# Optimization experiments

Hardware: AMD Instinct MI355X
Metric: run time of the kernel (lower is better)

## Reference

```python
import jax, jax.numpy as jnp
import numpy as np

N = 50000
E = 800000
H = 96
NUM_IN = 11
PE_DIM = 24
NUM_OUT = 1
NUM_LAYERS = 4
NUM_GRAPHS = 256


def _linear_params(key, d_in, d_out):
    k1, k2 = jax.random.split(key)
    bound = 1.0 / np.sqrt(d_in)
    w = jax.random.uniform(k1, (d_in, d_out), jnp.float32, -bound, bound)
    b = jax.random.uniform(k2, (d_out,), jnp.float32, -bound, bound)
    return w, b


def setup_inputs() -> dict:
    key = jax.random.key(0)
    ks = jax.random.split(key, 32)
    x = jax.random.normal(ks[0], (N, NUM_IN), jnp.float32)
    pos = jax.random.normal(ks[1], (N, 3), jnp.float32)
    pe = jax.random.normal(ks[2], (N, PE_DIM), jnp.float32)
    edge_index = jax.random.randint(ks[3], (2, E), 0, N, jnp.int64)
    batch = jnp.sort(jax.random.randint(ks[4], (N,), 0, NUM_GRAPHS, jnp.int64))
    embed_w1, embed_b1 = _linear_params(ks[5], NUM_IN + PE_DIM, H)
    embed_w2, embed_b2 = _linear_params(ks[6], H, H)
    # per-layer stacked params
    msg_w1 = []; msg_b1 = []; msg_w2 = []; msg_b2 = []
    upd_w1 = []; upd_b1 = []; upd_w2 = []; upd_b2 = []
    for l in range(NUM_LAYERS):
        w, b = _linear_params(ks[7 + l], 2 * H + 1, H); msg_w1.append(w); msg_b1.append(b)
        w, b = _linear_params(ks[11 + l], H, H); msg_w2.append(w); msg_b2.append(b)
        w, b = _linear_params(ks[15 + l], 2 * H, H); upd_w1.append(w); upd_b1.append(b)
        w, b = _linear_params(ks[19 + l], H, H); upd_w2.append(w); upd_b2.append(b)
    pre_w1, pre_b1 = _linear_params(ks[23], H, H)
    pre_w2, pre_b2 = _linear_params(ks[24], H, H)
    ro_w1, ro_b1 = _linear_params(ks[25], H, H)
    ro_w2, ro_b2 = _linear_params(ks[26], H, NUM_OUT)
    return {
        'x': x, 'pos': pos, 'pe': pe, 'edge_index': edge_index, 'batch': batch,
        'embed_w1': embed_w1, 'embed_b1': embed_b1, 'embed_w2': embed_w2, 'embed_b2': embed_b2,
        'msg_w1': jnp.stack(msg_w1), 'msg_b1': jnp.stack(msg_b1),
        'msg_w2': jnp.stack(msg_w2), 'msg_b2': jnp.stack(msg_b2),
        'upd_w1': jnp.stack(upd_w1), 'upd_b1': jnp.stack(upd_b1),
        'upd_w2': jnp.stack(upd_w2), 'upd_b2': jnp.stack(upd_b2),
        'pre_w1': pre_w1, 'pre_b1': pre_b1, 'pre_w2': pre_w2, 'pre_b2': pre_b2,
        'ro_w1': ro_w1, 'ro_b1': ro_b1, 'ro_w2': ro_w2, 'ro_b2': ro_b2,
    }


def _egnn_forward(x, pos, pe, edge_index, batch,
                  embed_w1, embed_b1, embed_w2, embed_b2,
                  msg_w1, msg_b1, msg_w2, msg_b2,
                  upd_w1, upd_b1, upd_w2, upd_b2,
                  pre_w1, pre_b1, pre_w2, pre_b2,
                  ro_w1, ro_b1, ro_w2, ro_b2):
    silu = jax.nn.silu
    send, rec = edge_index[0], edge_index[1]
    h = jnp.concatenate([x, pe], axis=-1)
    h = silu(h @ embed_w1 + embed_b1) @ embed_w2 + embed_b2  # [N,H]
    dist = jnp.linalg.norm(pos[send] - pos[rec], axis=1)[:, None]  # [E,1]
    for l in range(NUM_LAYERS):
        state = jnp.concatenate([h[send], h[rec], dist], axis=1)  # [E,2H+1]
        msg = silu(silu(state @ msg_w1[l] + msg_b1[l]) @ msg_w2[l] + msg_b2[l])  # [E,H]
        aggr = jax.ops.segment_sum(msg, rec, num_segments=h.shape[0])  # [N,H]
        upd_in = jnp.concatenate([h, aggr], axis=1)
        update = silu(upd_in @ upd_w1[l] + upd_b1[l]) @ upd_w2[l] + upd_b2[l]
        h = h + update
    h = silu(h @ pre_w1 + pre_b1) @ pre_w2 + pre_b2
    pooled = jax.ops.segment_sum(h, batch, num_segments=NUM_GRAPHS)  # [G,H]
    out = silu(pooled @ ro_w1 + ro_b1) @ ro_w2 + ro_b2  # [G,1]
    return jnp.squeeze(out)


def reference(x, pos, pe, edge_index, batch,
              embed_w1, embed_b1, embed_w2, embed_b2,
              msg_w1, msg_b1, msg_w2, msg_b2,
              upd_w1, upd_b1, upd_w2, upd_b2,
              pre_w1, pre_b1, pre_w2, pre_b2,
              ro_w1, ro_b1, ro_w2, ro_b2):
    return _egnn_forward(x, pos, pe, edge_index, batch,
                         embed_w1, embed_b1, embed_w2, embed_b2,
                         msg_w1, msg_b1, msg_w2, msg_b2,
                         upd_w1, upd_b1, upd_w2, upd_b2,
                         pre_w1, pre_b1, pre_w2, pre_b2,
                         ro_w1, ro_b1, ro_w2, ro_b2)
```

## Files before the change

kernel.cpp:

```cpp
#include <hip/hip_runtime.h>
#include <hip/hip_bf16.h>

#define HDIM 96
#define TILE 128

typedef __attribute__((ext_vector_type(8))) short  short8;
typedef __attribute__((ext_vector_type(4))) short  short4v;
typedef __attribute__((ext_vector_type(4))) float  float4v;
typedef __attribute__((ext_vector_type(4))) unsigned int uint4v;

static __device__ __forceinline__ short f2bf(float f){
    __hip_bfloat16 h = __float2bfloat16(f);
    return *reinterpret_cast<short*>(&h);
}
static __device__ __forceinline__ float bf2f(short s){
    unsigned u = ((unsigned)(unsigned short)s) << 16;
    return __uint_as_float(u);
}
static __device__ __forceinline__ float silu_f(float v){
    return v * __builtin_amdgcn_rcpf(1.0f + __expf(-v));
}

struct SwJob { const float* src; int ck; int ks; int ksrc; };
struct SwTable { SwJob j[22]; };

__global__ __launch_bounds__(256) void swizzle_kernel(SwTable T, short* __restrict__ dst, int total){
    int gid = blockIdx.x*256 + threadIdx.x;
    if (gid >= total) return;
    int ksg = gid / 3072;
    int e   = gid % 3072;
    const float* src = T.j[0].src; int k0 = 0, ksrc = 0;
    #pragma unroll
    for (int jj = 0; jj < 22; ++jj){
        int s = T.j[jj].ck;
        if (ksg >= s && ksg < s + T.j[jj].ks){ src = T.j[jj].src; k0 = (ksg - s)*32; ksrc = T.j[jj].ksrc; }
    }
    int nt   = e >> 9;
    int rem  = e & 511;
    int lane = rem >> 3;
    int jx   = rem & 7;
    int k = k0 + ((lane >> 4) << 3) + jx;
    int f = nt*16 + (lane & 15);
    float v = (k < ksrc) ? src[(size_t)k*HDIM + f] : 0.0f;
    dst[gid] = f2bf(v);
}

__global__ __launch_bounds__(256) void swizzle2_kernel(const float* __restrict__ msg_w1,
                                                       short* __restrict__ dst, int total){
    int gid = blockIdx.x*256 + threadIdx.x;
    if (gid >= total) return;
    int layer = gid / 18432;
    int e     = gid % 18432;
    int ksg = e / 6144;
    int rem = e % 6144;
    int nt   = rem >> 9;
    int r2   = rem & 511;
    int lane = r2 >> 3;
    int jx   = r2 & 7;
    int k = ksg*32 + ((lane >> 4) << 3) + jx;
    int f = nt*16 + (lane & 15);
    int row = (f < 96) ? k : (96 + k);
    int col = (f < 96) ? f : (f - 96);
    dst[gid] = f2bf(msg_w1[(size_t)layer*193*96 + (size_t)row*96 + col]);
}

__global__ __launch_bounds__(256) void hist_kernel(const int* __restrict__ rec, int* __restrict__ deg, int E){
    int e = blockIdx.x*256 + threadIdx.x;
    if (e < E) atomicAdd(&deg[rec[e]], 1);
}

__global__ __launch_bounds__(256) void scan_part(const int* __restrict__ deg, int* __restrict__ part, int N){
    __shared__ int red[256];
    const int t = threadIdx.x;
    int base = blockIdx.x*1024;
    int s = 0;
    #pragma unroll
    for (int j=0;j<4;j++){ int i = base + j*256 + t; s += (i<N)?deg[i]:0; }
    red[t]=s; __syncthreads();
    #pragma unroll
    for (int off=128; off>0; off>>=1){ if (t<off) red[t]+=red[t+off]; __syncthreads(); }
    if (t==0) part[blockIdx.x]=red[0];
}
__global__ void scan_top(int* __restrict__ part, int nb){
    if (threadIdx.x==0){ int run=0; for (int i=0;i<nb;i++){ int v=part[i]; part[i]=run; run+=v; } }
}
__global__ __launch_bounds__(256) void scan_final(const int* __restrict__ deg, const int* __restrict__ part,
                                                  int* __restrict__ cur, int N){
    __shared__ int tsum[256];
    const int t = threadIdx.x;
    int i0 = blockIdx.x*1024 + t*4;
    int a0 = (i0+0<N)?deg[i0+0]:0;
    int a1 = (i0+1<N)?deg[i0+1]:0;
    int a2 = (i0+2<N)?deg[i0+2]:0;
    int a3 = (i0+3<N)?deg[i0+3]:0;
    int s = a0+a1+a2+a3;
    tsum[t]=s; __syncthreads();
    #pragma unroll
    for (int off=1; off<256; off<<=1){
        int u = (t>=off)?tsum[t-off]:0;
        __syncthreads();
        tsum[t]+=u;
        __syncthreads();
    }
    int excl = tsum[t]-s + part[blockIdx.x];
    if (i0+0<N) cur[i0+0]=excl;
    if (i0+1<N) cur[i0+1]=excl+a0;
    if (i0+2<N) cur[i0+2]=excl+a0+a1;
    if (i0+3<N) cur[i0+3]=excl+a0+a1+a2;
}

__global__ __launch_bounds__(256) void scatter_kernel(
    const int* __restrict__ send, const int* __restrict__ rec, const float* __restrict__ pos,
    int* __restrict__ cur, int* __restrict__ send_s, int* __restrict__ rec_s,
    float* __restrict__ dist_s, int E)
{
    int e = blockIdx.x*256 + threadIdx.x;
    if (e >= E) return;
    int s = send[e], r = rec[e];
    int p = atomicAdd(&cur[r], 1);
    send_s[p] = s;
    rec_s[p]  = r;
    float dx = pos[3*s]   - pos[3*r];
    float dy = pos[3*s+1] - pos[3*r+1];
    float dz = pos[3*s+2] - pos[3*r+2];
    dist_s[p] = sqrtf(dx*dx + dy*dy + dz*dz);
}

__global__ __launch_bounds__(256,2) void msgpre_kernel(
    const short* __restrict__ hbf, const short* __restrict__ w1sr, const float* __restrict__ b1,
    short* __restrict__ SR, int N)
{
    __shared__ short stateS[TILE*104];
    const int t  = threadIdx.x;
    const int n0 = blockIdx.x * TILE;

    #pragma unroll
    for (int it = 0; it < 6; ++it) {
        int q = it*256 + t;
        int c = q % 12;
        int i = q / 12;
        int node = n0 + i;
        uint4v v = {0u,0u,0u,0u};
        if (node < N) v = *(const uint4v*)(hbf + (size_t)node*HDIM + c*8);
        *(uint4v*)(stateS + i*104 + c*8) = v;
    }
    __syncthreads();

    const int lane = t & 63;
    const int wv   = t >> 6;
    const int e_lo = wv * 32;
    const int col  = lane & 15;
    const int quad = lane >> 4;
    const int koff = quad * 8;
    const int frow = quad * 4;
    const float4v fzero = {0.f,0.f,0.f,0.f};

    float4v acc[2][12];
    #pragma unroll
    for (int i=0;i<2;i++)
      #pragma unroll
      for (int n=0;n<12;n++) acc[i][n] = fzero;

    const short8* w1f = (const short8*)w1sr;
    #pragma unroll
    for (int ks = 0; ks < 3; ++ks) {
        short8 bb0 = *(const short8*)(stateS + (e_lo+col)*104    + ks*32 + koff);
        short8 bb1 = *(const short8*)(stateS + (e_lo+16+col)*104 + ks*32 + koff);
        #pragma unroll
        for (int mt = 0; mt < 12; ++mt) {
            short8 a = w1f[(ks*12+mt)*64 + lane];
            acc[0][mt] = __builtin_amdgcn_mfma_f32_16x16x32_bf16(a, bb0, acc[0][mt], 0, 0, 0);
            acc[1][mt] = __builtin_amdgcn_mfma_f32_16x16x32_bf16(a, bb1, acc[1][mt], 0, 0, 0);
        }
    }
    float4v b1v[6];
    #pragma unroll
    for (int mt=0; mt<6; ++mt) b1v[mt] = *(const float4v*)(b1 + mt*16 + frow);

    #pragma unroll
    for (int et=0; et<2; ++et){
        int node = n0 + e_lo + et*16 + col;
        if (node < N) {
            size_t base = (size_t)node*192;
            #pragma unroll
            for (int mt=0; mt<12; ++mt){
                float4v o = acc[et][mt];
                if (mt < 6) { o[0]+=b1v[mt][0]; o[1]+=b1v[mt][1]; o[2]+=b1v[mt][2]; o[3]+=b1v[mt][3]; }
                short4v sv = {f2bf(o[0]), f2bf(o[1]), f2bf(o[2]), f2bf(o[3])};
                *(short4v*)(SR + base + mt*16 + frow) = sv;
            }
        }
    }
}

__global__ __launch_bounds__(256,3) void edge_kernel(
    const short* __restrict__ SR,
    const int* __restrict__ send_s, const int* __restrict__ rec_s, const float* __restrict__ dist_s,
    const float* __restrict__ w1r192,
    const short* __restrict__ w2sw, const float* __restrict__ b2,
    float* __restrict__ aggr, int E)
{
    __shared__ float msgS[TILE*100];
    __shared__ int   recS[TILE];
    __shared__ int   startIdxS[TILE+1];
    __shared__ int   wcntS[2];
    const int t  = threadIdx.x;
    const int e0 = blockIdx.x * TILE;

    if (t < TILE) {
        int e = e0 + t; if (e >= E) e = E - 1;
        recS[t] = rec_s[e];
    }
    __syncthreads();

    bool flag = false;
    if (t < TILE) flag = (t == 0) || (recS[t] != recS[t-1]);
    unsigned long long bmask = __ballot(flag ? 1 : 0);
    int pre = __popcll(bmask & ((1ull << (t & 63)) - 1ull));
    if (t < TILE && (t & 63) == 0) wcntS[t >> 6] = __popcll(bmask);
    __syncthreads();
    const int nseg = wcntS[0] + wcntS[1];
    if (flag) startIdxS[pre + ((t >> 6) ? wcntS[0] : 0)] = t;
    if (t == 0) startIdxS[nseg] = TILE;

    const int lane = t & 63;
    const int wv   = t >> 6;
    const int e_lo = wv * 32;
    const int col  = lane & 15;
    const int quad = lane >> 4;
    const int frow = quad * 4;
    const float4v fzero = {0.f,0.f,0.f,0.f};

    short8 frag[2][3];
    #pragma unroll
    for (int et=0; et<2; ++et){
        int ei = e_lo + et*16 + col;
        int ec = e0 + ei; if (ec >= E) ec = E - 1;
        int se = send_s[ec];
        int re = recS[ei];
        float d = dist_s[ec];
        #pragma unroll
        for (int ks=0; ks<3; ++ks){
            int f0 = ks*32 + quad*8;
            short8 S8 = *(const short8*)(SR + (size_t)se*192 + f0);
            short8 R8 = *(const short8*)(SR + (size_t)re*192 + 96 + f0);
            float4v wa = *(const float4v*)(w1r192 + f0);
            float4v wb = *(const float4v*)(w1r192 + f0 + 4);
            short8 fr;
            #pragma unroll
            for (int j=0;j<8;j++){
                float w = (j<4) ? wa[j] : wb[j-4];
                float v = bf2f(S8[j]) + bf2f(R8[j]) + d*w;
                fr[j] = f2bf(silu_f(v));
            }
            frag[et][ks] = fr;
        }
    }

    float4v acc2[2][6];
    #pragma unroll
    for (int i=0;i<2;i++)
      #pragma unroll
      for (int n=0;n<6;n++) acc2[i][n] = fzero;

    const short8* w2f = (const short8*)w2sw;
    #pragma unroll
    for (int ks = 0; ks < 3; ++ks) {
        #pragma unroll
        for (int mt = 0; mt < 6; ++mt) {
            short8 a = w2f[(ks*6+mt)*64 + lane];
            acc2[0][mt] = __builtin_amdgcn_mfma_f32_16x16x32_bf16(a, frag[0][ks], acc2[0][mt], 0, 0, 0);
            acc2[1][mt] = __builtin_amdgcn_mfma_f32_16x16x32_bf16(a, frag[1][ks], acc2[1][mt], 0, 0, 0);
        }
    }
    float4v b2v[6];
    #pragma unroll
    for (int mt=0; mt<6; ++mt) b2v[mt] = *(const float4v*)(b2 + mt*16 + frow);

    #pragma unroll
    for (int et=0; et<2; ++et){
        int e = e_lo + et*16 + col;
        bool valid = (e0 + e) < E;
        #pragma unroll
        for (int mt=0; mt<6; ++mt){
            float4v v;
            #pragma unroll
            for (int r=0;r<4;r++){
                float u = silu_f(acc2[et][mt][r] + b2v[mt][r]);
                v[r] = valid ? u : 0.0f;
            }
            *(float4v*)(msgS + e*100 + mt*16 + frow) = v;
        }
    }
    __syncthreads();

    const int items = nseg * 24;
    for (int item = t; item < items; item += 256){
        int s  = item / 24;
        int fg = item - s*24;
        int r0 = startIdxS[s], r1 = startIdxS[s+1];
        float4v sum = fzero;
        for (int r = r0; r < r1; ++r) sum += *(const float4v*)(msgS + r*100 + fg*4);
        float* dstp = aggr + (size_t)recS[r0]*HDIM + fg*4;
        atomicAdd(dstp+0, sum[0]);
        atomicAdd(dstp+1, sum[1]);
        atomicAdd(dstp+2, sum[2]);
        atomicAdd(dstp+3, sum[3]);
    }
}

__global__ __launch_bounds__(256,3) void update_kernel(
    float* __restrict__ h, short* __restrict__ hbf, float* __restrict__ aggr,
    const short* __restrict__ w1sw, const float* __restrict__ b1,
    const short* __restrict__ w2sw, const float* __restrict__ b2, int N)
{
    __shared__ short stateS[TILE*200];
    const int t  = threadIdx.x;
    const int n0 = blockIdx.x * TILE;

    #pragma unroll
    for (int it = 0; it < 12; ++it) {
        int q = it*256 + t;
        int c = q % 24;
        int i = q / 24;
        int node = n0 + i;
        if (c < 12) {
            uint4v v = {0u,0u,0u,0u};
            if (node < N) v = *(const uint4v*)(hbf + (size_t)node*HDIM + c*8);
            *(uint4v*)(stateS + i*200 + c*8) = v;
        } else {
            int cc = c - 12;
            short8 s8 = {0,0,0,0,0,0,0,0};
            if (node < N) {
                float4v a0 = *(const float4v*)(aggr + (size_t)node*HDIM + cc*8);
                float4v a1 = *(const float4v*)(aggr + (size_t)node*HDIM + cc*8 + 4);
                s8[0]=f2bf(a0[0]); s8[1]=f2bf(a0[1]); s8[2]=f2bf(a0[2]); s8[3]=f2bf(a0[3]);
                s8[4]=f2bf(a1[0]); s8[5]=f2bf(a1[1]); s8[6]=f2bf(a1[2]); s8[7]=f2bf(a1[3]);
            }
            *(short8*)(stateS + i*200 + HDIM + cc*8) = s8;
        }
    }
    __syncthreads();

    const int lane = t & 63;
    const int wv   = t >> 6;
    const int e_lo = wv * 32;
    const int col  = lane & 15;
    const int quad = lane >> 4;
    const int koff = quad * 8;
    const int frow = quad * 4;
    const float4v fzero = {0.f,0.f,0.f,0.f};

    float4v acc[2][6];
    #pragma unroll
    for (int i=0;i<2;i++)
      #pragma unroll
      for (int n=0;n<6;n++) acc[i][n] = fzero;

    const short8* w1f = (const short8*)w1sw;
    #pragma unroll
    for (int ks = 0; ks < 6; ++ks) {
        short8 bb0 = *(const short8*)(stateS + (e_lo+col)*200    + ks*32 + koff);
        short8 bb1 = *(const short8*)(stateS + (e_lo+16+col)*200 + ks*32 + koff);
        #pragma unroll
        for (int mt = 0; mt < 6; ++mt) {
            short8 a = w1f[(ks*6+mt)*64 + lane];
            acc[0][mt] = __builtin_amdgcn_mfma_f32_16x16x32_bf16(a, bb0, acc[0][mt], 0, 0, 0);
            acc[1][mt] = __builtin_amdgcn_mfma_f32_16x16x32_bf16(a, bb1, acc[1][mt], 0, 0, 0);
        }
    }
    float4v b1v[6];
    #pragma unroll
    for (int mt=0; mt<6; ++mt) b1v[mt] = *(const float4v*)(b1 + mt*16 + frow);
    __syncthreads();

    short* t1S = stateS;
    #pragma unroll
    for (int et=0; et<2; ++et){
        int e = e_lo + et*16 + col;
        #pragma unroll
        for (int mt=0; mt<6; ++mt){
            short4v sv;
            #pragma unroll
            for (int r=0;r<4;r++) sv[r] = f2bf(silu_f(acc[et][mt][r] + b1v[mt][r]));
            *(short4v*)(t1S + e*104 + mt*16 + frow) = sv;
        }
    }
    __syncthreads();

    float4v acc2[2][6];
    #pragma unroll
    for (int i=0;i<2;i++)
      #pragma unroll
      for (int n=0;n<6;n++) acc2[i][n] = fzero;

    const short8* w2f = (const short8*)w2sw;
    #pragma unroll
    for (int ks = 0; ks < 3; ++ks) {
        short8 bb0 = *(const short8*)(t1S + (e_lo+col)*104    + ks*32 + koff);
        short8 bb1 = *(const short8*)(t1S + (e_lo+16+col)*104 + ks*32 + koff);
        #pragma unroll
        for (int mt = 0; mt < 6; ++mt) {
            short8 a = w2f[(ks*6+mt)*64 + lane];
            acc2[0][mt] = __builtin_amdgcn_mfma_f32_16x16x32_bf16(a, bb0, acc2[0][mt], 0, 0, 0);
            acc2[1][mt] = __builtin_amdgcn_mfma_f32_16x16x32_bf16(a, bb1, acc2[1][mt], 0, 0, 0);
        }
    }
    float4v b2v[6];
    #pragma unroll
    for (int mt=0; mt<6; ++mt) b2v[mt] = *(const float4v*)(b2 + mt*16 + frow);

    #pragma unroll
    for (int et=0; et<2; ++et){
        int node = n0 + e_lo + et*16 + col;
        if (node < N) {
            size_t base = (size_t)node*HDIM;
            #pragma unroll
            for (int mt=0; mt<6; ++mt){
                int f0 = mt*16 + frow;
                float4v old = *(const float4v*)(h + base + f0);
                float4v o;
                #pragma unroll
                for (int r=0;r<4;r++) o[r] = old[r] + acc2[et][mt][r] + b2v[mt][r];
                *(float4v*)(h + base + f0) = o;
                short4v sv = {f2bf(o[0]), f2bf(o[1]), f2bf(o[2]), f2bf(o[3])};
                *(short4v*)(hbf + base + f0) = sv;
                *(float4v*)(aggr + base + f0) = fzero;
            }
        }
    }
}

__global__ __launch_bounds__(256,3) void embed_kernel(
    const float* __restrict__ x, const float* __restrict__ pe,
    const short* __restrict__ w1sw, const float* __restrict__ b1,
    const short* __restrict__ w2sw, const float* __restrict__ b2,
    float* __restrict__ h, short* __restrict__ hbf, int N)
{
    __shared__ short stateS[TILE*72];
    __shared__ short t1S[TILE*104];
    const int t  = threadIdx.x;
    const int n0 = blockIdx.x * TILE;

    if (t < TILE) {
        int node = n0 + t;
        short* row = stateS + t*72;
        if (node < N) {
            #pragma unroll
            for (int j=0;j<11;j++) row[j]    = f2bf(x[(size_t)node*11 + j]);
            #pragma unroll
            for (int j=0;j<24;j++) row[11+j] = f2bf(pe[(size_t)node*24 + j]);
            #pragma unroll
            for (int j=35;j<64;j++) row[j] = 0;
        } else {
            #pragma unroll
            for (int j=0;j<64;j++) row[j] = 0;
        }
    }
    __syncthreads();

    const int lane = t & 63;
    const int wv   = t >> 6;
    const int e_lo = wv * 32;
    const int col  = lane & 15;
    const int quad = lane >> 4;
    const int koff = quad * 8;
    const int frow = quad * 4;
    const float4v fzero = {0.f,0.f,0.f,0.f};

    float4v acc[2][6];
    #pragma unroll
    for (int i=0;i<2;i++)
      #pragma unroll
      for (int n=0;n<6;n++) acc[i][n] = fzero;

    const short8* w1f = (const short8*)w1sw;
    #pragma unroll
    for (int ks = 0; ks < 2; ++ks) {
        short8 bb0 = *(const short8*)(stateS + (e_lo+col)*72    + ks*32 + koff);
        short8 bb1 = *(const short8*)(stateS + (e_lo+16+col)*72 + ks*32 + koff);
        #pragma unroll
        for (int mt = 0; mt < 6; ++mt) {
            short8 a = w1f[(ks*6+mt)*64 + lane];
            acc[0][mt] = __builtin_amdgcn_mfma_f32_16x16x32_bf16(a, bb0, acc[0][mt], 0, 0, 0);
            acc[1][mt] = __builtin_amdgcn_mfma_f32_16x16x32_bf16(a, bb1, acc[1][mt], 0, 0, 0);
        }
    }
    float4v b1v[6];
    #pragma unroll
    for (int mt=0; mt<6; ++mt) b1v[mt] = *(const float4v*)(b1 + mt*16 + frow);

    #pragma unroll
    for (int et=0; et<2; ++et){
        int e = e_lo + et*16 + col;
        #pragma unroll
        for (int mt=0; mt<6; ++mt){
            short4v sv;
            #pragma unroll
            for (int r=0;r<4;r++) sv[r] = f2bf(silu_f(acc[et][mt][r] + b1v[mt][r]));
            *(short4v*)(t1S + e*104 + mt*16 + frow) = sv;
        }
    }
    __syncthreads();

    float4v acc2[2][6];
    #pragma unroll
    for (int i=0;i<2;i++)
      #pragma unroll
      for (int n=0;n<6;n++) acc2[i][n] = fzero;

    const short8* w2f = (const short8*)w2sw;
    #pragma unroll
    for (int ks = 0; ks < 3; ++ks) {
        short8 bb0 = *(const short8*)(t1S + (e_lo+col)*104    + ks*32 + koff);
        short8 bb1 = *(const short8*)(t1S + (e_lo+16+col)*104 + ks*32 + koff);
        #pragma unroll
        for (int mt = 0; mt < 6; ++mt) {
            short8 a = w2f[(ks*6+mt)*64 + lane];
            acc2[0][mt] = __builtin_amdgcn_mfma_f32_16x16x32_bf16(a, bb0, acc2[0][mt], 0, 0, 0);
            acc2[1][mt] = __builtin_amdgcn_mfma_f32_16x16x32_bf16(a, bb1, acc2[1][mt], 0, 0, 0);
        }
    }
    float4v b2v[6];
    #pragma unroll
    for (int mt=0; mt<6; ++mt) b2v[mt] = *(const float4v*)(b2 + mt*16 + frow);

    #pragma unroll
    for (int et=0; et<2; ++et){
        int node = n0 + e_lo + et*16 + col;
        if (node < N) {
            size_t base = (size_t)node*HDIM;
            #pragma unroll
            for (int mt=0; mt<6; ++mt){
                int f0 = mt*16 + frow;
                float4v o;
                #pragma unroll
                for (int r=0;r<4;r++) o[r] = acc2[et][mt][r] + b2v[mt][r];
                *(float4v*)(h + base + f0) = o;
                short4v sv = {f2bf(o[0]), f2bf(o[1]), f2bf(o[2]), f2bf(o[3])};
                *(short4v*)(hbf + base + f0) = sv;
            }
        }
    }
}

__global__ __launch_bounds__(256,2) void prepool_kernel(
    const short* __restrict__ hbf,
    const short* __restrict__ w1sw, const float* __restrict__ b1,
    const short* __restrict__ w2sw, const float* __restrict__ b2,
    const int* __restrict__ batch, float* __restrict__ pooled, int N)
{
    __shared__ short bufS[TILE*104*2];
    __shared__ int   batchS[TILE];
    __shared__ int   startIdxS[TILE+1];
    __shared__ int   wcntS[2];
    short* stateS = bufS;
    short* t1S    = bufS + TILE*104;
    float* msgS   = (float*)bufS;
    const int t  = threadIdx.x;
    const int n0 = blockIdx.x * TILE;

    #pragma unroll
    for (int it = 0; it < 6; ++it) {
        int q = it*256 + t;
        int c = q % 12;
        int i = q / 12;
        int node = n0 + i;
        uint4v v = {0u,0u,0u,0u};
        if (node < N) v = *(const uint4v*)(hbf + (size_t)node*HDIM + c*8);
        *(uint4v*)(stateS + i*104 + c*8) = v;
    }
    if (t < TILE) {
        int node = n0 + t;
        batchS[t] = batch[node < N ? node : N-1];
    }
    __syncthreads();

    bool flag = false;
    if (t < TILE) flag = (t == 0) || (batchS[t] != batchS[t-1]);
    unsigned long long bmask = __ballot(flag ? 1 : 0);
    int pre = __popcll(bmask & ((1ull << (t & 63)) - 1ull));
    if (t < TILE && (t & 63) == 0) wcntS[t >> 6] = __popcll(bmask);

    const int lane = t & 63;
    const int wv   = t >> 6;
    const int e_lo = wv * 32;
    const int col  = lane & 15;
    const int quad = lane >> 4;
    const int koff = quad * 8;
    const int frow = quad * 4;
    const float4v fzero = {0.f,0.f,0.f,0.f};

    float4v acc[2][6];
    #pragma unroll
    for (int i=0;i<2;i++)
      #pragma unroll
      for (int n=0;n<6;n++) acc[i][n] = fzero;

    const short8* w1f = (const short8*)w1sw;
    #pragma unroll
    for (int ks = 0; ks < 3; ++ks) {
        short8 bb0 = *(const short8*)(stateS + (e_lo+col)*104    + ks*32 + koff);
        short8 bb1 = *(const short8*)(stateS + (e_lo+16+col)*104 + ks*32 + koff);
        #pragma unroll
        for (int mt = 0; mt < 6; ++mt) {
            short8 a = w1f[(ks*6+mt)*64 + lane];
            acc[0][mt] = __builtin_amdgcn_mfma_f32_16x16x32_bf16(a, bb0, acc[0][mt], 0, 0, 0);
            acc[1][mt] = __builtin_amdgcn_mfma_f32_16x16x32_bf16(a, bb1, acc[1][mt], 0, 0, 0);
        }
    }
    float4v b1v[6];
    #pragma unroll
    for (int mt=0; mt<6; ++mt) b1v[mt] = *(const float4v*)(b1 + mt*16 + frow);

    #pragma unroll
    for (int et=0; et<2; ++et){
        int e = e_lo + et*16 + col;
        #pragma unroll
        for (int mt=0; mt<6; ++mt){
            short4v sv;
            #pragma unroll
            for (int r=0;r<4;r++) sv[r] = f2bf(silu_f(acc[et][mt][r] + b1v[mt][r]));
            *(short4v*)(t1S + e*104 + mt*16 + frow) = sv;
        }
    }
    __syncthreads();
    const int nseg = wcntS[0] + wcntS[1];
    if (flag) startIdxS[pre + ((t >> 6) ? wcntS[0] : 0)] = t;
    if (t == 0) startIdxS[nseg] = TILE;

    float4v acc2[2][6];
    #pragma unroll
    for (int i=0;i<2;i++)
      #pragma unroll
      for (int n=0;n<6;n++) acc2[i][n] = fzero;

    const short8* w2f = (const short8*)w2sw;
    #pragma unroll
    for (int ks = 0; ks < 3; ++ks) {
        short8 bb0 = *(const short8*)(t1S + (e_lo+col)*104    + ks*32 + koff);
        short8 bb1 = *(const short8*)(t1S + (e_lo+16+col)*104 + ks*32 + koff);
        #pragma unroll
        for (int mt = 0; mt < 6; ++mt) {
            short8 a = w2f[(ks*6+mt)*64 + lane];
            acc2[0][mt] = __builtin_amdgcn_mfma_f32_16x16x32_bf16(a, bb0, acc2[0][mt], 0, 0, 0);
            acc2[1][mt] = __builtin_amdgcn_mfma_f32_16x16x32_bf16(a, bb1, acc2[1][mt], 0, 0, 0);
        }
    }
    float4v b2v[6];
    #pragma unroll
    for (int mt=0; mt<6; ++mt) b2v[mt] = *(const float4v*)(b2 + mt*16 + frow);
    __syncthreads();

    #pragma unroll
    for (int et=0; et<2; ++et){
        int e = e_lo + et*16 + col;
        bool valid = (n0 + e) < N;
        #pragma unroll
        for (int mt=0; mt<6; ++mt){
            float4v v;
            #pragma unroll
            for (int r=0;r<4;r++){
                float u = acc2[et][mt][r] + b2v[mt][r];
                v[r] = valid ? u : 0.0f;
            }
            *(float4v*)(msgS + e*100 + mt*16 + frow) = v;
        }
    }
    __syncthreads();

    const int items = nseg * 24;
    for (int item = t; item < items; item += 256){
        int s  = item / 24;
        int fg = item - s*24;
        int r0 = startIdxS[s], r1 = startIdxS[s+1];
        float4v sum = fzero;
        for (int r = r0; r < r1; ++r) sum += *(const float4v*)(msgS + r*100 + fg*4);
        float* dstp = pooled + (size_t)batchS[r0]*HDIM + fg*4;
        atomicAdd(dstp+0, sum[0]);
        atomicAdd(dstp+1, sum[1]);
        atomicAdd(dstp+2, sum[2]);
        atomicAdd(dstp+3, sum[3]);
    }
}

__global__ __launch_bounds__(128) void readout_kernel(
    const float* __restrict__ pooled,
    const float* __restrict__ w1, const float* __restrict__ b1,
    const float* __restrict__ w2, const float* __restrict__ b2,
    float* __restrict__ out)
{
    __shared__ float red[128];
    const int g = blockIdx.x;
    const int t = threadIdx.x;
    float p = 0.0f;
    if (t < HDIM) {
        float acc = b1[t];
        for (int k = 0; k < HDIM; ++k)
            acc += pooled[(size_t)g*HDIM + k] * w1[(size_t)k*HDIM + t];
        acc = silu_f(acc);
        p = acc * w2[t];
    }
    red[t] = p;
    __syncthreads();
    for (int s = 64; s > 0; s >>= 1) {
        if (t < s) red[t] += red[t + s];
        __syncthreads();
    }
    if (t == 0) out[g] = red[0] + b2[0];
}

extern "C" void kernel_launch(void* const* d_in, const int* in_sizes, int n_in,
                              void* d_out, int out_size, void* d_ws, size_t ws_size,
                              hipStream_t stream)
{
    const float* x        = (const float*)d_in[0];
    const float* pos      = (const float*)d_in[1];
    const float* pe       = (const float*)d_in[2];
    const int*   ei       = (const int*)d_in[3];
    const int*   batch    = (const int*)d_in[4];
    const float* embed_w1 = (const float*)d_in[5];
    const float* embed_b1 = (const float*)d_in[6];
    const float* embed_w2 = (const float*)d_in[7];
    const float* embed_b2 = (const float*)d_in[8];
    const float* msg_w1   = (const float*)d_in[9];
    const float* msg_b1   = (const float*)d_in[10];
    const float* msg_w2   = (const float*)d_in[11];
    const float* msg_b2   = (const float*)d_in[12];
    const float* upd_w1   = (const float*)d_in[13];
    const float* upd_b1   = (const float*)d_in[14];
    const float* upd_w2   = (const float*)d_in[15];
    const float* upd_b2   = (const float*)d_in[16];
    const float* pre_w1   = (const float*)d_in[17];
    const float* pre_b1   = (const float*)d_in[18];
    const float* pre_w2   = (const float*)d_in[19];
    const float* pre_b2   = (const float*)d_in[20];
    const float* ro_w1    = (const float*)d_in[21];
    const float* ro_b1    = (const float*)d_in[22];
    const float* ro_w2    = (const float*)d_in[23];
    const float* ro_b2    = (const float*)d_in[24];

    const int E = in_sizes[3] / 2;
    const int N = in_sizes[4];
    const int G = out_size;

    char* ws = (char*)d_ws;
    size_t off = 0;
    auto alloc = [&](size_t bytes){ void* p = ws + off; off += (bytes + 255) & ~(size_t)255; return p; };
    float* h      = (float*)alloc((size_t)N*HDIM*4);
    short* hbf    = (short*)alloc((size_t)N*HDIM*2);
    float* aggr   = (float*)alloc((size_t)N*HDIM*4);
    float* pooled = (float*)alloc((size_t)G*HDIM*4);
    short* wsw    = (short*)alloc((size_t)59*3072*2);
    short* w1sr   = (short*)alloc((size_t)4*18432*2);
    short* SR     = (short*)alloc((size_t)N*192*2);
    int*   deg    = (int*)alloc((size_t)N*4);
    int*   cur    = (int*)alloc((size_t)N*4);
    int*   part   = (int*)alloc((size_t)256*4);
    int*   send_s = (int*)alloc((size_t)E*4);
    int*   rec_s  = (int*)alloc((size_t)E*4);
    float* dist_s = (float*)alloc((size_t)E*4);

    hipMemsetAsync(aggr,   0, (size_t)N*HDIM*4, stream);
    hipMemsetAsync(pooled, 0, (size_t)G*HDIM*4, stream);
    hipMemsetAsync(deg,    0, (size_t)N*4, stream);

    SwTable T;
    for (int jj=0;jj<22;jj++){ T.j[jj].src = embed_w1; T.j[jj].ck = 1<<30; T.j[jj].ks = 0; T.j[jj].ksrc = 0; }
    int ck = 0, ji = 0;
    auto add = [&](const float* s, int ks, int ksrc){
        T.j[ji].src = s; T.j[ji].ck = ck; T.j[ji].ks = ks; T.j[ji].ksrc = ksrc;
        ji++; ck += ks;
    };
    add(embed_w1, 2, 35);
    add(embed_w2, 3, 96);
    add(pre_w1,   3, 96);
    add(pre_w2,   3, 96);
    for (int l=0;l<4;l++) add(msg_w2 + (size_t)l*96*96,  3, 96);
    for (int l=0;l<4;l++) add(upd_w1 + (size_t)l*192*96, 6, 192);
    for (int l=0;l<4;l++) add(upd_w2 + (size_t)l*96*96,  3, 96);
    const int total = 59*3072;
    swizzle_kernel<<<(total+255)/256, 256, 0, stream>>>(T, wsw, total);
    const int total2 = 4*18432;
    swizzle2_kernel<<<(total2+255)/256, 256, 0, stream>>>(msg_w1, w1sr, total2);

    const int nbE256 = (E + 255) / 256;
    const int nbScan = (N + 1023) / 1024;
    hist_kernel<<<nbE256, 256, 0, stream>>>(ei + E, deg, E);
    scan_part<<<nbScan, 256, 0, stream>>>(deg, part, N);
    scan_top<<<1, 64, 0, stream>>>(part, nbScan);
    scan_final<<<nbScan, 256, 0, stream>>>(deg, part, cur, N);
    scatter_kernel<<<nbE256, 256, 0, stream>>>(ei, ei + E, pos, cur, send_s, rec_s, dist_s, E);

    const int nbN = (N + TILE - 1) / TILE;
    embed_kernel<<<nbN, 256, 0, stream>>>(x, pe, wsw + 0, embed_b1, wsw + 2*3072, embed_b2, h, hbf, N);

    const int nbE = (E + TILE - 1) / TILE;
    for (int l = 0; l < 4; ++l) {
        msgpre_kernel<<<nbN, 256, 0, stream>>>(hbf, w1sr + (size_t)l*18432, msg_b1 + l*96, SR, N);
        edge_kernel<<<nbE, 256, 0, stream>>>(SR, send_s, rec_s, dist_s,
            msg_w1 + (size_t)l*193*96 + (size_t)192*96,
            wsw + (11 + 3*l)*3072, msg_b2 + l*96, aggr, E);
        update_kernel<<<nbN, 256, 0, stream>>>(h, hbf, aggr,
            wsw + (23 + 6*l)*3072, upd_b1 + l*96,
            wsw + (47 + 3*l)*3072, upd_b2 + l*96, N);
    }

    prepool_kernel<<<nbN, 256, 0, stream>>>(hbf, wsw + 5*3072, pre_b1, wsw + 8*3072, pre_b2,
                                            batch, pooled, N);
    readout_kernel<<<G, 128, 0, stream>>>(pooled, ro_w1, ro_b1, ro_w2, ro_b2, (float*)d_out);
}
```

Baseline: 823.7 us.

## Fuse message pre-projection into update/embed kernels, bf16 edge staging, parallel scan

Removes the separate msgpre kernel: the next layer's sender/receiver projection (SR) is computed in the epilogue of update_kernel, and in embed_kernel for layer 0, from the freshly written bf16 node state held in shared memory. This saves a launch per layer and a re-read of hbf. The edge kernel now stages messages in LDS as bf16 instead of fp32, shrinking shared memory so occupancy can rise to 5 blocks per CU, and each item reduces 8 features. scan_top becomes a parallel 256-thread Hillis-Steele scan instead of a single-thread loop. Risks include bf16 rounding of messages before aggregation, higher register pressure in the fused update kernel, and a scan that assumes at most 256 partial blocks.

```diff
diff --git a/kernel.cpp b/kernel.cpp
--- a/kernel.cpp
+++ b/kernel.cpp
@@ -81,8 +81,20 @@
     for (int off=128; off>0; off>>=1){ if (t<off) red[t]+=red[t+off]; __syncthreads(); }
     if (t==0) part[blockIdx.x]=red[0];
 }
-__global__ void scan_top(int* __restrict__ part, int nb){
-    if (threadIdx.x==0){ int run=0; for (int i=0;i<nb;i++){ int v=part[i]; part[i]=run; run+=v; } }
+__global__ __launch_bounds__(256) void scan_top(int* __restrict__ part, int nb){
+    __shared__ int buf[256];
+    const int t = threadIdx.x;
+    int v = (t < nb) ? part[t] : 0;
+    buf[t] = v;
+    __syncthreads();
+    #pragma unroll
+    for (int off=1; off<256; off<<=1){
+        int u = (t>=off)?buf[t-off]:0;
+        __syncthreads();
+        buf[t] += u;
+        __syncthreads();
+    }
+    if (t < nb) part[t] = buf[t] - v;
 }
 __global__ __launch_bounds__(256) void scan_final(const int* __restrict__ deg, const int* __restrict__ part,
                                                   int* __restrict__ cur, int N){
@@ -126,81 +138,14 @@
     dist_s[p] = sqrtf(dx*dx + dy*dy + dz*dz);
 }
 
-__global__ __launch_bounds__(256,2) void msgpre_kernel(
-    const short* __restrict__ hbf, const short* __restrict__ w1sr, const float* __restrict__ b1,
-    short* __restrict__ SR, int N)
-{
-    __shared__ short stateS[TILE*104];
-    const int t  = threadIdx.x;
-    const int n0 = blockIdx.x * TILE;
-
-    #pragma unroll
-    for (int it = 0; it < 6; ++it) {
-        int q = it*256 + t;
-        int c = q % 12;
-        int i = q / 12;
-        int node = n0 + i;
-        uint4v v = {0u,0u,0u,0u};
-        if (node < N) v = *(const uint4v*)(hbf + (size_t)node*HDIM + c*8);
-        *(uint4v*)(stateS + i*104 + c*8) = v;
-    }
-    __syncthreads();
-
-    const int lane = t & 63;
-    const int wv   = t >> 6;
-    const int e_lo = wv * 32;
-    const int col  = lane & 15;
-    const int quad = lane >> 4;
-    const int koff = quad * 8;
-    const int frow = quad * 4;
-    const float4v fzero = {0.f,0.f,0.f,0.f};
-
-    float4v acc[2][12];
-    #pragma unroll
-    for (int i=0;i<2;i++)
-      #pragma unroll
-      for (int n=0;n<12;n++) acc[i][n] = fzero;
-
-    const short8* w1f = (const short8*)w1sr;
-    #pragma unroll
-    for (int ks = 0; ks < 3; ++ks) {
-        short8 bb0 = *(const short8*)(stateS + (e_lo+col)*104    + ks*32 + koff);
-        short8 bb1 = *(const short8*)(stateS + (e_lo+16+col)*104 + ks*32 + koff);
-        #pragma unroll
-        for (int mt = 0; mt < 12; ++mt) {
-            short8 a = w1f[(ks*12+mt)*64 + lane];
-            acc[0][mt] = __builtin_amdgcn_mfma_f32_16x16x32_bf16(a, bb0, acc[0][mt], 0, 0, 0);
-            acc[1][mt] = __builtin_amdgcn_mfma_f32_16x16x32_bf16(a, bb1, acc[1][mt], 0, 0, 0);
-        }
-    }
-    float4v b1v[6];
-    #pragma unroll
-    for (int mt=0; mt<6; ++mt) b1v[mt] = *(const float4v*)(b1 + mt*16 + frow);
-
-    #pragma unroll
-    for (int et=0; et<2; ++et){
-        int node = n0 + e_lo + et*16 + col;
-        if (node < N) {
-            size_t base = (size_t)node*192;
-            #pragma unroll
-            for (int mt=0; mt<12; ++mt){
-                float4v o = acc[et][mt];
-                if (mt < 6) { o[0]+=b1v[mt][0]; o[1]+=b1v[mt][1]; o[2]+=b1v[mt][2]; o[3]+=b1v[mt][3]; }
-                short4v sv = {f2bf(o[0]), f2bf(o[1]), f2bf(o[2]), f2bf(o[3])};
-                *(short4v*)(SR + base + mt*16 + frow) = sv;
-            }
-        }
-    }
-}
-
-__global__ __launch_bounds__(256,3) void edge_kernel(
+__global__ __launch_bounds__(256,5) void edge_kernel(
     const short* __restrict__ SR,
     const int* __restrict__ send_s, const int* __restrict__ rec_s, const float* __restrict__ dist_s,
     const float* __restrict__ w1r192,
     const short* __restrict__ w2sw, const float* __restrict__ b2,
     float* __restrict__ aggr, int E)
 {
-    __shared__ float msgS[TILE*100];
+    __shared__ short msgS[TILE*104];
     __shared__ int   recS[TILE];
     __shared__ int   startIdxS[TILE+1];
     __shared__ int   wcntS[2];
@@ -283,36 +228,40 @@
         bool valid = (e0 + e) < E;
         #pragma unroll
         for (int mt=0; mt<6; ++mt){
-            float4v v;
+            short4v sv;
             #pragma unroll
             for (int r=0;r<4;r++){
                 float u = silu_f(acc2[et][mt][r] + b2v[mt][r]);
-                v[r] = valid ? u : 0.0f;
+                sv[r] = f2bf(valid ? u : 0.0f);
             }
-            *(float4v*)(msgS + e*100 + mt*16 + frow) = v;
-        }
-    }
-    __syncthreads();
-
-    const int items = nseg * 24;
+            *(short4v*)(msgS + e*104 + mt*16 + frow) = sv;
+        }
+    }
+    __syncthreads();
+
+    const int items = nseg * 12;
     for (int item = t; item < items; item += 256){
-        int s  = item / 24;
-        int fg = item - s*24;
+        int s  = item / 12;
+        int fg = item - s*12;
         int r0 = startIdxS[s], r1 = startIdxS[s+1];
-        float4v sum = fzero;
-        for (int r = r0; r < r1; ++r) sum += *(const float4v*)(msgS + r*100 + fg*4);
-        float* dstp = aggr + (size_t)recS[r0]*HDIM + fg*4;
-        atomicAdd(dstp+0, sum[0]);
-        atomicAdd(dstp+1, sum[1]);
-        atomicAdd(dstp+2, sum[2]);
-        atomicAdd(dstp+3, sum[3]);
+        float sum[8] = {0.f,0.f,0.f,0.f,0.f,0.f,0.f,0.f};
+        for (int r = r0; r < r1; ++r){
+            short8 v8 = *(const short8*)(msgS + r*104 + fg*8);
+            #pragma unroll
+            for (int j=0;j<8;j++) sum[j] += bf2f(v8[j]);
+        }
+        float* dstp = aggr + (size_t)recS[r0]*HDIM + fg*8;
+        #pragma unroll
+        for (int j=0;j<8;j++) atomicAdd(dstp+j, sum[j]);
     }
 }
 
 __global__ __launch_bounds__(256,3) void update_kernel(
     float* __restrict__ h, short* __restrict__ hbf, float* __restrict__ aggr,
     const short* __restrict__ w1sw, const float* __restrict__ b1,
-    const short* __restrict__ w2sw, const float* __restrict__ b2, int N)
+    const short* __restrict__ w2sw, const float* __restrict__ b2,
+    const short* __restrict__ w1sr_next, const float* __restrict__ msgb1_next,
+    short* __restrict__ SR, int N)
 {
     __shared__ short stateS[TILE*200];
     const int t  = threadIdx.x;
@@ -409,23 +358,67 @@
     float4v b2v[6];
     #pragma unroll
     for (int mt=0; mt<6; ++mt) b2v[mt] = *(const float4v*)(b2 + mt*16 + frow);
+    __syncthreads();
 
     #pragma unroll
     for (int et=0; et<2; ++et){
-        int node = n0 + e_lo + et*16 + col;
-        if (node < N) {
-            size_t base = (size_t)node*HDIM;
-            #pragma unroll
-            for (int mt=0; mt<6; ++mt){
-                int f0 = mt*16 + frow;
-                float4v old = *(const float4v*)(h + base + f0);
-                float4v o;
-                #pragma unroll
-                for (int r=0;r<4;r++) o[r] = old[r] + acc2[et][mt][r] + b2v[mt][r];
+        int erow = e_lo + et*16 + col;
+        int node = n0 + erow;
+        bool valid = node < N;
+        size_t base = (size_t)node*HDIM;
+        #pragma unroll
+        for (int mt=0; mt<6; ++mt){
+            int f0 = mt*16 + frow;
+            float4v old = valid ? *(const float4v*)(h + base + f0) : fzero;
+            float4v o;
+            #pragma unroll
+            for (int r=0;r<4;r++) o[r] = old[r] + acc2[et][mt][r] + b2v[mt][r];
+            short4v sv = {f2bf(o[0]), f2bf(o[1]), f2bf(o[2]), f2bf(o[3])};
+            if (valid) {
                 *(float4v*)(h + base + f0) = o;
-                short4v sv = {f2bf(o[0]), f2bf(o[1]), f2bf(o[2]), f2bf(o[3])};
                 *(short4v*)(hbf + base + f0) = sv;
                 *(float4v*)(aggr + base + f0) = fzero;
+            }
+            *(short4v*)(stateS + erow*104 + f0) = sv;
+        }
+    }
+
+    if (w1sr_next) {
+        __syncthreads();
+        float4v accS[2][12];
+        #pragma unroll
+        for (int i=0;i<2;i++)
+          #pragma unroll
+          for (int n=0;n<12;n++) accS[i][n] = fzero;
+
+        const short8* wsf = (const short8*)w1sr_next;
+        #pragma unroll
+        for (int ks = 0; ks < 3; ++ks) {
+            short8 bb0 = *(const short8*)(stateS + (e_lo+col)*104    + ks*32 + koff);
+            short8 bb1 = *(const short8*)(stateS + (e_lo+16+col)*104 + ks*32 + koff);
+            #pragma unroll
+            for (int mt = 0; mt < 12; ++mt) {
+                short8 a = wsf[(ks*12+mt)*64 + lane];
+                accS[0][mt] = __builtin_amdgcn_mfma_f32_16x16x32_bf16(a, bb0, accS[0][mt], 0, 0, 0);
+                accS[1][mt] = __builtin_amdgcn_mfma_f32_16x16x32_bf16(a, bb1, accS[1][mt], 0, 0, 0);
+            }
+        }
+        float4v bnv[6];
+        #pragma unroll
+        for (int mt=0; mt<6; ++mt) bnv[mt] = *(const float4v*)(msgb1_next + mt*16 + frow);
+
+        #pragma unroll
+        for (int et=0; et<2; ++et){
+            int node = n0 + e_lo + et*16 + col;
+            if (node < N) {
+                size_t sbase = (size_t)node*192;
+                #pragma unroll
+                for (int mt=0; mt<12; ++mt){
+                    float4v o = accS[et][mt];
+                    if (mt < 6) { o[0]+=bnv[mt][0]; o[1]+=bnv[mt][1]; o[2]+=bnv[mt][2]; o[3]+=bnv[mt][3]; }
+                    short4v sv = {f2bf(o[0]), f2bf(o[1]), f2bf(o[2]), f2bf(o[3])};
+                    *(short4v*)(SR + sbase + mt*16 + frow) = sv;
+                }
             }
         }
     }
@@ -435,7 +428,9 @@
     const float* __restrict__ x, const float* __restrict__ pe,
     const short* __restrict__ w1sw, const float* __restrict__ b1,
     const short* __restrict__ w2sw, const float* __restrict__ b2,
-    float* __restrict__ h, short* __restrict__ hbf, int N)
+    float* __restrict__ h, short* __restrict__ hbf,
+    const short* __restrict__ w1sr0, const float* __restrict__ msgb1_0,
+    short* __restrict__ SR, int N)
 {
     __shared__ short stateS[TILE*72];
     __shared__ short t1S[TILE*104];
@@ -524,21 +519,63 @@
     float4v b2v[6];
     #pragma unroll
     for (int mt=0; mt<6; ++mt) b2v[mt] = *(const float4v*)(b2 + mt*16 + frow);
+    __syncthreads();
+
+    #pragma unroll
+    for (int et=0; et<2; ++et){
+        int erow = e_lo + et*16 + col;
+        int node = n0 + erow;
+        bool valid = node < N;
+        size_t base = (size_t)node*HDIM;
+        #pragma unroll
+        for (int mt=0; mt<6; ++mt){
+            int f0 = mt*16 + frow;
+            float4v o;
+            #pragma unroll
+            for (int r=0;r<4;r++) o[r] = acc2[et][mt][r] + b2v[mt][r];
+            short4v sv = {f2bf(o[0]), f2bf(o[1]), f2bf(o[2]), f2bf(o[3])};
+            if (valid) {
+                *(float4v*)(h + base + f0) = o;
+                *(short4v*)(hbf + base + f0) = sv;
+            }
+            *(short4v*)(t1S + erow*104 + f0) = sv;
+        }
+    }
+    __syncthreads();
+
+    float4v accS[2][12];
+    #pragma unroll
+    for (int i=0;i<2;i++)
+      #pragma unroll
+      for (int n=0;n<12;n++) accS[i][n] = fzero;
+
+    const short8* wsf = (const short8*)w1sr0;
+    #pragma unroll
+    for (int ks = 0; ks < 3; ++ks) {
+        short8 bb0 = *(const short8*)(t1S + (e_lo+col)*104    + ks*32 + koff);
+        short8 bb1 = *(const short8*)(t1S + (e_lo+16+col)*104 + ks*32 + koff);
+        #pragma unroll
+        for (int mt = 0; mt < 12; ++mt) {
+            short8 a = wsf[(ks*12+mt)*64 + lane];
+            accS[0][mt] = __builtin_amdgcn_mfma_f32_16x16x32_bf16(a, bb0, accS[0][mt], 0, 0, 0);
+            accS[1][mt] = __builtin_amdgcn_mfma_f32_16x16x32_bf16(a, bb1, accS[1][mt], 0, 0, 0);
+        }
+    }
+    float4v bnv[6];
+    #pragma unroll
+    for (int mt=0; mt<6; ++mt) bnv[mt] = *(const float4v*)(msgb1_0 + mt*16 + frow);
 
     #pragma unroll
     for (int et=0; et<2; ++et){
         int node = n0 + e_lo + et*16 + col;
         if (node < N) {
-            size_t base = (size_t)node*HDIM;
-            #pragma unroll
-            for (int mt=0; mt<6; ++mt){
-                int f0 = mt*16 + frow;
-                float4v o;
-                #pragma unroll
-                for (int r=0;r<4;r++) o[r] = acc2[et][mt][r] + b2v[mt][r];
-                *(float4v*)(h + base + f0) = o;
+            size_t sbase = (size_t)node*192;
+            #pragma unroll
+            for (int mt=0; mt<12; ++mt){
+                float4v o = accS[et][mt];
+                if (mt < 6) { o[0]+=bnv[mt][0]; o[1]+=bnv[mt][1]; o[2]+=bnv[mt][2]; o[3]+=bnv[mt][3]; }
                 short4v sv = {f2bf(o[0]), f2bf(o[1]), f2bf(o[2]), f2bf(o[3])};
-                *(short4v*)(hbf + base + f0) = sv;
+                *(short4v*)(SR + sbase + mt*16 + frow) = sv;
             }
         }
     }
@@ -788,22 +825,25 @@
     const int nbScan = (N + 1023) / 1024;
     hist_kernel<<<nbE256, 256, 0, stream>>>(ei + E, deg, E);
     scan_part<<<nbScan, 256, 0, stream>>>(deg, part, N);
-    scan_top<<<1, 64, 0, stream>>>(part, nbScan);
+    scan_top<<<1, 256, 0, stream>>>(part, nbScan);
     scan_final<<<nbScan, 256, 0, stream>>>(deg, part, cur, N);
     scatter_kernel<<<nbE256, 256, 0, stream>>>(ei, ei + E, pos, cur, send_s, rec_s, dist_s, E);
 
     const int nbN = (N + TILE - 1) / TILE;
-    embed_kernel<<<nbN, 256, 0, stream>>>(x, pe, wsw + 0, embed_b1, wsw + 2*3072, embed_b2, h, hbf, N);
+    embed_kernel<<<nbN, 256, 0, stream>>>(x, pe, wsw + 0, embed_b1, wsw + 2*3072, embed_b2,
+                                          h, hbf, w1sr, msg_b1, SR, N);
 
     const int nbE = (E + TILE - 1) / TILE;
     for (int l = 0; l < 4; ++l) {
-        msgpre_kernel<<<nbN, 256, 0, stream>>>(hbf, w1sr + (size_t)l*18432, msg_b1 + l*96, SR, N);
         edge_kernel<<<nbE, 256, 0, stream>>>(SR, send_s, rec_s, dist_s,
             msg_w1 + (size_t)l*193*96 + (size_t)192*96,
             wsw + (11 + 3*l)*3072, msg_b2 + l*96, aggr, E);
+        const short* w1sr_next = (l < 3) ? (w1sr + (size_t)(l+1)*18432) : nullptr;
+        const float* msgb1_next = (l < 3) ? (msg_b1 + (l+1)*96) : nullptr;
         update_kernel<<<nbN, 256, 0, stream>>>(h, hbf, aggr,
             wsw + (23 + 6*l)*3072, upd_b1 + l*96,
-            wsw + (47 + 3*l)*3072, upd_b2 + l*96, N);
+            wsw + (47 + 3*l)*3072, upd_b2 + l*96,
+            w1sr_next, msgb1_next, SR, N);
     }
 
     prepool_kernel<<<nbN, 256, 0, stream>>>(hbf, wsw + 5*3072, pre_b1, wsw + 8*3072, pre_b2,
```

Measured after the change: 1.105 ms. +34.1%, slower.
